# Performance work log

Measured on AMD Instinct MI355X. Metric: run time of the kernel, lower is better.

The kernel has to match this reference:

```python
import jax, jax.numpy as jnp
import numpy as np

EMBED = 1024
HEADS = 16
HEAD_DIM = EMBED // HEADS
FFN_DIM = 4096
SEQ = 2048
BATCH = 2
EPS = 1e-5


def setup_inputs() -> dict:
    key = jax.random.key(0)
    ks = jax.random.split(key, 13)
    s = lambda n: 1.0 / np.sqrt(n)
    return {
        "x": jax.random.normal(ks[0], (BATCH, SEQ, EMBED), jnp.float32),
        # qkv projection (stored as [in, out])
        "w_qkv": jax.random.normal(ks[1], (EMBED, 3 * EMBED), jnp.float32) * s(EMBED),
        "b_qkv": jax.random.normal(ks[2], (3 * EMBED,), jnp.float32) * 0.02,
        "w_out": jax.random.normal(ks[3], (EMBED, EMBED), jnp.float32) * s(EMBED),
        "b_out": jax.random.normal(ks[4], (EMBED,), jnp.float32) * 0.02,
        # FFN
        "w_up": jax.random.normal(ks[5], (EMBED, FFN_DIM), jnp.float32) * s(EMBED),
        "b_up": jax.random.normal(ks[6], (FFN_DIM,), jnp.float32) * 0.02,
        "w_down": jax.random.normal(ks[7], (FFN_DIM, EMBED), jnp.float32) * s(FFN_DIM),
        "b_down": jax.random.normal(ks[8], (EMBED,), jnp.float32) * 0.02,
        # LayerNorms
        "g1": jnp.ones((EMBED,), jnp.float32),
        "be1": jnp.zeros((EMBED,), jnp.float32),
        "g2": jnp.ones((EMBED,), jnp.float32),
        "be2": jnp.zeros((EMBED,), jnp.float32),
    }


def _layernorm(x, g, b):
    mu = jnp.mean(x, axis=-1, keepdims=True)
    var = jnp.mean(jnp.square(x - mu), axis=-1, keepdims=True)
    return (x - mu) * jax.lax.rsqrt(var + EPS) * g + b


def reference(x, w_qkv, b_qkv, w_out, b_out, w_up, b_up, w_down, b_down, g1, be1, g2, be2):
    B, S, E = x.shape
    qkv = (x @ w_qkv + b_qkv).reshape(B, S, 3, HEADS, HEAD_DIM)
    qkv = jnp.transpose(qkv, (2, 0, 3, 1, 4))
    q, k, v = qkv[0], qkv[1], qkv[2]
    scale = 1.0 / jnp.sqrt(jnp.float32(HEAD_DIM))
    attn = jnp.einsum("bhqd,bhkd->bhqk", q, k) * scale  # [B,H,S,S]
    causal = jnp.tril(jnp.ones((S, S), bool))
    attn = jnp.where(causal, attn, -jnp.inf)
    attn = jax.nn.softmax(attn, axis=-1)
    out = jnp.einsum("bhqk,bhkd->bhqd", attn, v)  # [B,H,S,D]
    out = jnp.transpose(out, (0, 2, 1, 3)).reshape(B, S, E)
    attn_out = out @ w_out + b_out
    x = _layernorm(x + attn_out, g1, be1)
    ffn_out = jax.nn.relu(x @ w_up + b_up) @ w_down + b_down
    return _layernorm(x + ffn_out, g2, be2)
```

## Files before the change

### kernel.cpp

```cpp
#include <hip/hip_runtime.h>
#include <hip/hip_bf16.h>

#define EMBED 1024
#define HEADS 16
#define HDIM 64
#define FFN 4096
#define SEQ 2048
#define BATCH 2
#define MTOT (BATCH*SEQ)
#define QSCALE 0.1803368801111137f

typedef __attribute__((ext_vector_type(8))) short bf16x8;
typedef __attribute__((ext_vector_type(4))) float f32x4;
typedef __attribute__((ext_vector_type(16))) float f32x16;
typedef unsigned short u16;
typedef unsigned int u32;

__device__ __forceinline__ u16 f2bf(float f) {
  union { float f; unsigned u; } v; v.f = f;
  unsigned r = v.u + 0x7FFFu + ((v.u >> 16) & 1u);
  return (u16)(r >> 16);
}

__device__ __forceinline__ void async_ld16(const void* g, void* l) {
  __builtin_amdgcn_global_load_lds((const __attribute__((address_space(1))) void*)g,
                                   (__attribute__((address_space(3))) void*)l,
                                   16, 0, 0);
}

__global__ __launch_bounds__(256) void k_cvt(const float* __restrict__ in,
                                             u16* __restrict__ out, int n4) {
  int i = blockIdx.x * 256 + threadIdx.x;
  int st = gridDim.x * 256;
  for (; i < n4; i += st) {
    float4 v = ((const float4*)in)[i];
    ushort4 o;
    o.x = f2bf(v.x); o.y = f2bf(v.y); o.z = f2bf(v.z); o.w = f2bf(v.w);
    ((ushort4*)out)[i] = o;
  }
}

__global__ __launch_bounds__(256) void k_tr(const float* __restrict__ w,
                                            u16* __restrict__ wT, int K, int N) {
  __shared__ u16 tile[32][33];
  int n0 = blockIdx.x * 32, k0 = blockIdx.y * 32;
  int tx = threadIdx.x, ty = threadIdx.y;
  #pragma unroll
  for (int i = 0; i < 4; ++i) {
    int k = k0 + ty + i * 8;
    tile[ty + i * 8][tx] = f2bf(w[(size_t)k * N + n0 + tx]);
  }
  __syncthreads();
  #pragma unroll
  for (int i = 0; i < 4; ++i) {
    int n = n0 + ty + i * 8;
    wT[(size_t)n * K + k0 + tx] = tile[tx][ty + i * 8];
  }
}

__global__ __launch_bounds__(256) void k_vtr(const u16* __restrict__ V,
                                             u16* __restrict__ Vt) {
  __shared__ u16 t[64][72];
  const int s0 = blockIdx.x * 64;
  const size_t ib = (size_t)blockIdx.y * (size_t)SEQ * HDIM;
  const size_t ob = (size_t)blockIdx.y * (size_t)HDIM * SEQ;
  const int tid = threadIdx.x;
  const int r = tid >> 2, c0 = (tid & 3) * 16;
  bf16x8 v0 = *(const bf16x8*)(V + ib + (size_t)(s0 + r) * HDIM + c0);
  bf16x8 v1 = *(const bf16x8*)(V + ib + (size_t)(s0 + r) * HDIM + c0 + 8);
  #pragma unroll
  for (int j = 0; j < 8; ++j) {
    t[c0 + j][r] = (u16)v0[j];
    t[c0 + 8 + j][r] = (u16)v1[j];
  }
  __syncthreads();
  const int d = tid >> 2, sc = (tid & 3) * 16;
  bf16x8 o0, o1;
  #pragma unroll
  for (int j = 0; j < 8; ++j) { o0[j] = t[d][sc + j]; o1[j] = t[d][sc + 8 + j]; }
  *(bf16x8*)(Vt + ob + (size_t)d * SEQ + s0 + sc) = o0;
  *(bf16x8*)(Vt + ob + (size_t)d * SEQ + s0 + sc + 8) = o1;
}

template <int OMODE, bool RELU>
__global__ __launch_bounds__(512) void k_gemm8(
    const u16* __restrict__ A, const u16* __restrict__ BT,
    const float* __restrict__ bias,
    void* __restrict__ out0, void* __restrict__ out1, void* __restrict__ out2,
    int M, int N, int K) {
  __shared__ __align__(16) u16 As[2][2][128 * 64];
  __shared__ __align__(16) u16 Bs[2][2][128 * 64];
  const int tid = threadIdx.x;
  const int lane = tid & 63, g = lane >> 4, li = lane & 15;
  const int wid = tid >> 6, wm = wid >> 2, wn = wid & 3;

  const int gx = gridDim.x;
  const int nwg = gx * gridDim.y;
  const int flat = blockIdx.y * gx + blockIdx.x;
  const int cpx = nwg >> 3;
  const int swz = (flat & 7) * cpx + (flat >> 3);
  const int m0 = (swz / gx) * 256, n0 = (swz % gx) * 256;

  f32x4 acc[8][4] = {};

  const u16* Ablk = A + (size_t)m0 * K;
  const u16* Bblk = BT + (size_t)n0 * K;
  const int trow = tid >> 3;
  const int sc = (tid & 7) ^ (trow & 7);

  auto stageA = [&](int buf, int h, int kt) {
    #pragma unroll
    for (int r = 0; r < 2; ++r)
      async_ld16(Ablk + (size_t)(h * 64 + r * 128 + trow) * K + kt + sc * 8,
                 &As[buf][h][0] + r * 4096 + tid * 8);
  };
  auto stageB = [&](int buf, int h, int kt) {
    #pragma unroll
    for (int r = 0; r < 2; ++r) {
      const int p = trow + r * 64;
      async_ld16(Bblk + (size_t)(((p >> 5) << 6) + h * 32 + (p & 31)) * K + kt + sc * 8,
                 &Bs[buf][h][0] + r * 4096 + tid * 8);
    }
  };

#define VM4_ asm volatile("s_waitcnt vmcnt(4)" ::: "memory")
#define VM2_ asm volatile("s_waitcnt vmcnt(2)" ::: "memory")
#define VM0_ asm volatile("s_waitcnt vmcnt(0)" ::: "memory")
#define VMN_
#define GP8(IH, JH, VMSTMT, STAGE_STMT) do {                                   \
    bf16x8 a_[4][2], b_[2][2];                                                 \
    _Pragma("unroll")                                                          \
    for (int i2 = 0; i2 < 4; ++i2) {                                           \
      const int pa = wm * 64 + i2 * 16 + li;                                   \
      _Pragma("unroll")                                                        \
      for (int ks = 0; ks < 2; ++ks)                                           \
        a_[i2][ks] = *(const bf16x8*)(&As[cur][IH][0] + pa * 64 +              \
                                      (((ks * 4 + g) ^ (li & 7)) * 8));        \
    }                                                                          \
    _Pragma("unroll")                                                          \
    for (int j2 = 0; j2 < 2; ++j2) {                                           \
      const int pb = wn * 32 + j2 * 16 + li;                                   \
      _Pragma("unroll")                                                        \
      for (int ks = 0; ks < 2; ++ks)                                           \
        b_[j2][ks] = *(const bf16x8*)(&Bs[cur][JH][0] + pb * 64 +              \
                                      (((ks * 4 + g) ^ (li & 7)) * 8));        \
    }                                                                          \
    STAGE_STMT;                                                                \
    VMSTMT;                                                                    \
    __builtin_amdgcn_s_barrier();                                              \
    asm volatile("s_waitcnt lgkmcnt(0)" ::: "memory");                         \
    __builtin_amdgcn_sched_barrier(0);                                         \
    __builtin_amdgcn_s_setprio(1);                                             \
    _Pragma("unroll")                                                          \
    for (int ks = 0; ks < 2; ++ks)                                             \
      _Pragma("unroll")                                                        \
      for (int i2 = 0; i2 < 4; ++i2)                                           \
        _Pragma("unroll")                                                      \
        for (int j2 = 0; j2 < 2; ++j2)                                         \
          acc[IH * 4 + i2][JH * 2 + j2] = __builtin_amdgcn_mfma_f32_16x16x32_bf16( \
              a_[i2][ks], b_[j2][ks], acc[IH * 4 + i2][JH * 2 + j2], 0, 0, 0); \
    __builtin_amdgcn_s_setprio(0);                                             \
    __builtin_amdgcn_s_barrier();                                              \
    asm volatile("" ::: "memory");                                             \
  } while (0)

  stageA(0, 0, 0); stageB(0, 0, 0); stageA(0, 1, 0); stageB(0, 1, 0);
  VM4_;
  __builtin_amdgcn_s_barrier();
  asm volatile("" ::: "memory");

  int cur = 0;
  const int nkt = K >> 6;
  for (int t = 0; t < nkt - 1; ++t) {
    const int kn = (t + 1) * 64;
    GP8(0, 0, VM4_, stageA(cur ^ 1, 0, kn));
    GP8(1, 0, VM4_, stageB(cur ^ 1, 0, kn));
    GP8(0, 1, VMN_, stageA(cur ^ 1, 1, kn));
    GP8(1, 1, VM4_, stageB(cur ^ 1, 1, kn));
    cur ^= 1;
  }
  GP8(0, 0, VM2_, );
  GP8(1, 0, VM0_, );
  GP8(0, 1, VMN_, );
  GP8(1, 1, VMN_, );
#undef GP8
#undef VM4_
#undef VM2_
#undef VM0_
#undef VMN_

  float bcol[4];
  #pragma unroll
  for (int j = 0; j < 4; ++j) bcol[j] = bias[n0 + wn * 64 + j * 16 + li];

  #pragma unroll
  for (int i = 0; i < 8; ++i) {
    #pragma unroll
    for (int j = 0; j < 4; ++j) {
      #pragma unroll
      for (int r = 0; r < 4; ++r) {
        int row = m0 + wm * 128 + i * 16 + g * 4 + r;
        int col = n0 + wn * 64 + j * 16 + li;
        float v = acc[i][j][r] + bcol[j];
        if (RELU) v = fmaxf(v, 0.f);
        if (OMODE == 0) {
          ((u16*)out0)[(size_t)row * N + col] = f2bf(v);
        } else {
          int which = col >> 10, hh = (col >> 6) & 15, d = col & 63;
          int bb = row >> 11, ss = row & 2047;
          if (which == 0) v *= QSCALE;
          u16* dst = which == 0 ? (u16*)out0 : (which == 1 ? (u16*)out1 : (u16*)out2);
          dst[((size_t)((bb * 16 + hh) * 2048 + ss)) * 64 + d] = f2bf(v);
        }
      }
    }
  }
}

template <int BN, int BK, int OMODE, bool RELU>
__global__ __launch_bounds__(256) void k_gemm(
    const u16* __restrict__ A, const u16* __restrict__ BT,
    const float* __restrict__ bias,
    void* __restrict__ out0, void* __restrict__ out1, void* __restrict__ out2,
    int M, int N, int K) {
  constexpr int NR = BN / 32;
  constexpr int KS = BK / 32;
  constexpr int TPR = BK / 8;
  constexpr int RPI = 256 / TPR;
  constexpr int CM = TPR - 1;

  __shared__ u16 As[2][128 * BK];
  __shared__ u16 Bs[2][BN * BK];
  const int tid = threadIdx.x;
  const int lane = tid & 63, g = lane >> 4, li = lane & 15;
  const int wid = tid >> 6, wm = wid >> 1, wn = wid & 1;

  const int gx = gridDim.x;
  const int nwg = gx * gridDim.y;
  const int flat = blockIdx.y * gx + blockIdx.x;
  const int cpx = nwg >> 3;
  const int swz = (flat & 7) * cpx + (flat >> 3);
  const int m0 = (swz / gx) * 128, n0 = (swz % gx) * BN;

  f32x4 acc[4][NR] = {};

  const u16* Ablk = A + (size_t)m0 * K;
  const u16* Bblk = BT + (size_t)n0 * K;
  const int srow = tid / TPR;
  const int scol = ((tid % TPR) ^ (srow & CM)) * 8;

  auto stage = [&](int buf, int kt) {
    #pragma unroll
    for (int r = 0; r < 128; r += RPI)
      async_ld16(Ablk + (size_t)(srow + r) * K + kt + scol, &As[buf][(srow + r) * BK] + (tid % TPR) * 8);
    #pragma unroll
    for (int r = 0; r < BN; r += RPI)
      async_ld16(Bblk + (size_t)(srow + r) * K + kt + scol, &Bs[buf][(srow + r) * BK] + (tid % TPR) * 8);
  };

  stage(0, 0);
  int cur = 0;
  for (int kt = 0; kt < K; kt += BK) {
    __syncthreads();
    if (kt + BK < K) stage(cur ^ 1, kt + BK);

    bf16x8 af[4][KS], bfr[NR][KS];
    #pragma unroll
    for (int i = 0; i < 4; ++i) {
      const int row = wm * 64 + i * 16 + li;
      #pragma unroll
      for (int ks = 0; ks < KS; ++ks) {
        const int c = ks * 4 + g;
        af[i][ks] = *(const bf16x8*)(&As[cur][row * BK] + ((c ^ (row & CM)) & CM) * 8);
      }
    }
    #pragma unroll
    for (int j = 0; j < NR; ++j) {
      const int row = wn * (BN / 2) + j * 16 + li;
      #pragma unroll
      for (int ks = 0; ks < KS; ++ks) {
        const int c = ks * 4 + g;
        bfr[j][ks] = *(const bf16x8*)(&Bs[cur][row * BK] + ((c ^ (row & CM)) & CM) * 8);
      }
    }
    #pragma unroll
    for (int ks = 0; ks < KS; ++ks)
      #pragma unroll
      for (int i = 0; i < 4; ++i)
        #pragma unroll
        for (int j = 0; j < NR; ++j)
          acc[i][j] = __builtin_amdgcn_mfma_f32_16x16x32_bf16(af[i][ks], bfr[j][ks], acc[i][j], 0, 0, 0);
    cur ^= 1;
  }

  float bcol[NR];
  #pragma unroll
  for (int j = 0; j < NR; ++j) bcol[j] = bias[n0 + wn * (BN / 2) + j * 16 + li];

  #pragma unroll
  for (int i = 0; i < 4; ++i) {
    #pragma unroll
    for (int j = 0; j < NR; ++j) {
      #pragma unroll
      for (int r = 0; r < 4; ++r) {
        int row = m0 + wm * 64 + i * 16 + g * 4 + r;
        int col = n0 + wn * (BN / 2) + j * 16 + li;
        float v = acc[i][j][r] + bcol[j];
        if (RELU) v = fmaxf(v, 0.f);
        if (OMODE == 0) {
          ((u16*)out0)[(size_t)row * N + col] = f2bf(v);
        } else if (OMODE == 1) {
          ((float*)out0)[(size_t)row * N + col] = v;
        } else {
          int which = col >> 10, hh = (col >> 6) & 15, d = col & 63;
          int bb = row >> 11, ss = row & 2047;
          if (which == 0) v *= QSCALE;
          u16* dst = which == 0 ? (u16*)out0 : (which == 1 ? (u16*)out1 : (u16*)out2);
          dst[((size_t)((bb * 16 + hh) * 2048 + ss)) * 64 + d] = f2bf(v);
        }
      }
    }
  }
}

__global__ __launch_bounds__(256, 3) void k_attn6(
    const u16* __restrict__ Q, const u16* __restrict__ K,
    const u16* __restrict__ Vt, u16* __restrict__ ctx) {
  const int bh = blockIdx.x;
  const int t32 = 63 - (int)blockIdx.y;
  const int b = bh >> 4, h = bh & 15;
  const int tid = threadIdx.x;
  const int wid = tid >> 6, lane = tid & 63;
  const int ql = lane & 31, hl = lane >> 5;

  __shared__ __align__(16) float mrg[3][64][34];

  const int wq0 = t32 * 32;
  const int qg = wq0 + ql;
  const int nt = ((wq0 + 31) >> 6) + 1;

  const size_t kbase = (size_t)bh * SEQ * HDIM;
  const size_t vbase = (size_t)bh * HDIM * SEQ;

  bf16x8 qf[4];
  #pragma unroll
  for (int d4 = 0; d4 < 4; ++d4)
    qf[d4] = *(const bf16x8*)(Q + kbase + (size_t)qg * HDIM + d4 * 16 + hl * 8);

  const u16* kp = K + kbase + (size_t)ql * HDIM + hl * 8;
  const u16* vp = Vt + vbase + (size_t)ql * SEQ + hl * 8;

  f32x16 o0 = {}, o1 = {};
  float m_run = -1e30f, l_run = 0.f;

  for (int kt = wid; kt < nt; kt += 4) {
    const bool kh1 = (kt * 64 + 32 <= wq0 + 31);
    const bool domask = (kt * 64 + (kh1 ? 63 : 31) > wq0);
    const int koff = kt * 64 * HDIM;

    bf16x8 kf0[4], kf1[4];
    #pragma unroll
    for (int d4 = 0; d4 < 4; ++d4) {
      kf0[d4] = *(const bf16x8*)(kp + koff + d4 * 16);
      if (kh1) kf1[d4] = *(const bf16x8*)(kp + koff + 32 * HDIM + d4 * 16);
    }
    bf16x8 vf0[4], vf1[4];
    #pragma unroll
    for (int t = 0; t < 4; ++t)
      if (t < 2 || kh1) {
        vf0[t] = *(const bf16x8*)(vp + kt * 64 + t * 16);
        vf1[t] = *(const bf16x8*)(vp + 32 * SEQ + kt * 64 + t * 16);
      }

    f32x16 S0 = {}, S1 = {};
    #pragma unroll
    for (int d4 = 0; d4 < 4; ++d4)
      S0 = __builtin_amdgcn_mfma_f32_32x32x16_bf16(kf0[d4], qf[d4], S0, 0, 0, 0);
    if (kh1) {
      #pragma unroll
      for (int d4 = 0; d4 < 4; ++d4)
        S1 = __builtin_amdgcn_mfma_f32_32x32x16_bf16(kf1[d4], qf[d4], S1, 0, 0, 0);
    }

    if (domask) {
      const int qrel = qg - kt * 64 - 4 * hl;
      #pragma unroll
      for (int r = 0; r < 16; ++r) {
        const int kc = (r & 3) + 8 * (r >> 2);
        S0[r] = (kc <= qrel) ? S0[r] : -3.0e38f;
      }
      if (kh1) {
        #pragma unroll
        for (int r = 0; r < 16; ++r) {
          const int kc = 32 + (r & 3) + 8 * (r >> 2);
          S1[r] = (kc <= qrel) ? S1[r] : -3.0e38f;
        }
      }
    }

    float mt = -3.0e38f;
    #pragma unroll
    for (int r = 0; r < 16; ++r) mt = fmaxf(mt, S0[r]);
    if (kh1) {
      #pragma unroll
      for (int r = 0; r < 16; ++r) mt = fmaxf(mt, S1[r]);
    }
    mt = fmaxf(mt, __shfl_xor(mt, 32, 64));

    if (!__all(mt <= m_run + 8.0f)) {
      const float mn = fmaxf(m_run, mt);
      const float alpha = exp2f(m_run - mn);
      l_run *= alpha;
      o0 *= alpha;
      o1 *= alpha;
      m_run = mn;
    }
    float sum = 0.f;
    #pragma unroll
    for (int r = 0; r < 16; ++r) { S0[r] = exp2f(S0[r] - m_run); sum += S0[r]; }
    if (kh1) {
      #pragma unroll
      for (int r = 0; r < 16; ++r) { S1[r] = exp2f(S1[r] - m_run); sum += S1[r]; }
    }
    sum += __shfl_xor(sum, 32, 64);
    l_run += sum;

    u32 pk[2][8], sw[2][8];
    #pragma unroll
    for (int m = 0; m < 4; ++m) {
      asm("v_cvt_pk_bf16_f32 %0, %1, %2" : "=v"(pk[0][2*m])   : "v"(S0[4*m+0]), "v"(S0[4*m+1]));
      asm("v_cvt_pk_bf16_f32 %0, %1, %2" : "=v"(pk[0][2*m+1]) : "v"(S0[4*m+2]), "v"(S0[4*m+3]));
    }
    #pragma unroll
    for (int i = 0; i < 8; ++i) sw[0][i] = __shfl_xor(pk[0][i], 32, 64);
    if (kh1) {
      #pragma unroll
      for (int m = 0; m < 4; ++m) {
        asm("v_cvt_pk_bf16_f32 %0, %1, %2" : "=v"(pk[1][2*m])   : "v"(S1[4*m+0]), "v"(S1[4*m+1]));
        asm("v_cvt_pk_bf16_f32 %0, %1, %2" : "=v"(pk[1][2*m+1]) : "v"(S1[4*m+2]), "v"(S1[4*m+3]));
      }
      #pragma unroll
      for (int i = 0; i < 8; ++i) sw[1][i] = __shfl_xor(pk[1][i], 32, 64);
    }

    #pragma unroll
    for (int t = 0; t < 4; ++t) {
      if (t < 2 || kh1) {
        const int c = t >> 1, m0 = 2 * (t & 1), m1 = m0 + 1;
        union { u32 u[4]; bf16x8 v; } pf;
        pf.u[0] = hl ? sw[c][2*m1]   : pk[c][2*m0];
        pf.u[1] = hl ? sw[c][2*m1+1] : pk[c][2*m0+1];
        pf.u[2] = hl ? pk[c][2*m1]   : sw[c][2*m0];
        pf.u[3] = hl ? pk[c][2*m1+1] : sw[c][2*m0+1];
        o0 = __builtin_amdgcn_mfma_f32_32x32x16_bf16(vf0[t], pf.v, o0, 0, 0, 0);
        o1 = __builtin_amdgcn_mfma_f32_32x32x16_bf16(vf1[t], pf.v, o1, 0, 0, 0);
      }
    }
  }

  if (wid > 0) {
    float* p = &mrg[wid - 1][lane][0];
    *(f32x16*)(p) = o0;
    *(f32x16*)(p + 16) = o1;
    p[32] = m_run;
    p[33] = l_run;
  }
  __syncthreads();
  if (wid > 0) return;

  float M = m_run;
  #pragma unroll
  for (int w = 0; w < 3; ++w) M = fmaxf(M, mrg[w][lane][32]);
  const float fa = exp2f(m_run - M);
  f32x16 acc0 = o0 * fa, acc1 = o1 * fa;
  float L = l_run * fa;
  #pragma unroll
  for (int w = 0; w < 3; ++w) {
    const float* p = &mrg[w][lane][0];
    const float fw = exp2f(p[32] - M);
    L += p[33] * fw;
    f32x16 t0 = *(const f32x16*)(p);
    f32x16 t1 = *(const f32x16*)(p + 16);
    acc0 += t0 * fw;
    acc1 += t1 * fw;
  }
  const float inv = 1.f / L;

  u16* outp = ctx + (size_t)(b * SEQ + qg) * EMBED + h * HDIM + 4 * hl;
  #pragma unroll
  for (int m = 0; m < 4; ++m) {
    ushort4 s0v, s1v;
    s0v.x = f2bf(acc0[4*m+0] * inv); s0v.y = f2bf(acc0[4*m+1] * inv);
    s0v.z = f2bf(acc0[4*m+2] * inv); s0v.w = f2bf(acc0[4*m+3] * inv);
    *(ushort4*)(outp + 8 * m) = s0v;
    s1v.x = f2bf(acc1[4*m+0] * inv); s1v.y = f2bf(acc1[4*m+1] * inv);
    s1v.z = f2bf(acc1[4*m+2] * inv); s1v.w = f2bf(acc1[4*m+3] * inv);
    *(ushort4*)(outp + 32 + 8 * m) = s1v;
  }
}

__global__ __launch_bounds__(256) void k_add_ln(
    const float* __restrict__ a, const float* __restrict__ bmat,
    const float* __restrict__ gam, const float* __restrict__ bet,
    float* __restrict__ outf, u16* __restrict__ outb) {
  const int row = blockIdx.x;
  const int t = threadIdx.x;
  __shared__ float red[8];
  float4 va = ((const float4*)(a + (size_t)row * EMBED))[t];
  float4 vb = ((const float4*)(bmat + (size_t)row * EMBED))[t];
  float s0 = va.x + vb.x, s1 = va.y + vb.y, s2 = va.z + vb.z, s3 = va.w + vb.w;
  float sum = s0 + s1 + s2 + s3;
  float sq = s0 * s0 + s1 * s1 + s2 * s2 + s3 * s3;
  #pragma unroll
  for (int m = 1; m < 64; m <<= 1) {
    sum += __shfl_xor(sum, m, 64);
    sq += __shfl_xor(sq, m, 64);
  }
  int wid = t >> 6;
  if ((t & 63) == 0) { red[wid] = sum; red[4 + wid] = sq; }
  __syncthreads();
  sum = red[0] + red[1] + red[2] + red[3];
  sq = red[4] + red[5] + red[6] + red[7];
  float mean = sum * (1.f / EMBED);
  float var = sq * (1.f / EMBED) - mean * mean;
  float rstd = rsqrtf(var + 1e-5f);
  float4 gv = ((const float4*)gam)[t], bev = ((const float4*)bet)[t];
  float y0 = (s0 - mean) * rstd * gv.x + bev.x;
  float y1 = (s1 - mean) * rstd * gv.y + bev.y;
  float y2 = (s2 - mean) * rstd * gv.z + bev.z;
  float y3 = (s3 - mean) * rstd * gv.w + bev.w;
  float4 o; o.x = y0; o.y = y1; o.z = y2; o.w = y3;
  ((float4*)(outf + (size_t)row * EMBED))[t] = o;
  if (outb) {
    ushort4 ob; ob.x = f2bf(y0); ob.y = f2bf(y1); ob.z = f2bf(y2); ob.w = f2bf(y3);
    ((ushort4*)(outb + (size_t)row * EMBED))[t] = ob;
  }
}

extern "C" void kernel_launch(void* const* d_in, const int* in_sizes, int n_in,
                              void* d_out, int out_size, void* d_ws, size_t ws_size,
                              hipStream_t stream) {
  const float* x      = (const float*)d_in[0];
  const float* w_qkv  = (const float*)d_in[1];
  const float* b_qkv  = (const float*)d_in[2];
  const float* w_out  = (const float*)d_in[3];
  const float* b_out  = (const float*)d_in[4];
  const float* w_up   = (const float*)d_in[5];
  const float* b_up   = (const float*)d_in[6];
  const float* w_down = (const float*)d_in[7];
  const float* b_down = (const float*)d_in[8];
  const float* g1  = (const float*)d_in[9];
  const float* be1 = (const float*)d_in[10];
  const float* g2  = (const float*)d_in[11];
  const float* be2 = (const float*)d_in[12];

  char* ws = (char*)d_ws;
  size_t off = 0;
  auto alloc = [&](size_t bytes) { void* p = ws + off; off += (bytes + 255) & ~(size_t)255; return p; };

  u16* xb     = (u16*)alloc((size_t)MTOT * EMBED * 2);
  u16* wqkvT  = (u16*)alloc((size_t)3 * EMBED * EMBED * 2);
  u16* woutT  = (u16*)alloc((size_t)EMBED * EMBED * 2);
  u16* wupT   = (u16*)alloc((size_t)FFN * EMBED * 2);
  u16* wdownT = (u16*)alloc((size_t)EMBED * FFN * 2);
  u16* qb     = (u16*)alloc((size_t)MTOT * EMBED * 2);
  u16* kb     = (u16*)alloc((size_t)MTOT * EMBED * 2);
  u16* vb     = (u16*)alloc((size_t)MTOT * EMBED * 2);
  u16* vtb    = (u16*)alloc((size_t)MTOT * EMBED * 2);
  u16* ctx    = (u16*)alloc((size_t)MTOT * EMBED * 2);
  float* attn_proj = (float*)alloc((size_t)MTOT * EMBED * 4);
  float* y_f32     = (float*)alloc((size_t)MTOT * EMBED * 4);
  u16* y_bf16      = (u16*)alloc((size_t)MTOT * EMBED * 2);
  u16* hmid        = (u16*)alloc((size_t)MTOT * FFN * 2);
  float* ffn_o     = (float*)alloc((size_t)MTOT * EMBED * 4);

  dim3 trb(32, 8);
  k_cvt<<<2048, 256, 0, stream>>>(x, xb, MTOT * EMBED / 4);
  k_tr<<<dim3(3 * EMBED / 32, EMBED / 32), trb, 0, stream>>>(w_qkv, wqkvT, EMBED, 3 * EMBED);
  k_tr<<<dim3(EMBED / 32, EMBED / 32), trb, 0, stream>>>(w_out, woutT, EMBED, EMBED);
  k_tr<<<dim3(FFN / 32, EMBED / 32), trb, 0, stream>>>(w_up, wupT, EMBED, FFN);
  k_tr<<<dim3(EMBED / 32, FFN / 32), trb, 0, stream>>>(w_down, wdownT, FFN, EMBED);

  k_gemm8<2, false><<<dim3(3 * EMBED / 256, MTOT / 256), 512, 0, stream>>>(
      xb, wqkvT, b_qkv, qb, kb, vb, MTOT, 3 * EMBED, EMBED);

  k_vtr<<<dim3(SEQ / 64, BATCH * HEADS), 256, 0, stream>>>(vb, vtb);

  k_attn6<<<dim3(BATCH * HEADS, 64), 256, 0, stream>>>(qb, kb, vtb, ctx);

  k_gemm<64, 64, 1, false><<<dim3(EMBED / 64, MTOT / 128), 256, 0, stream>>>(
      ctx, woutT, b_out, attn_proj, nullptr, nullptr, MTOT, EMBED, EMBED);

  k_add_ln<<<MTOT, 256, 0, stream>>>(x, attn_proj, g1, be1, y_f32, y_bf16);

  k_gemm8<0, true><<<dim3(FFN / 256, MTOT / 256), 512, 0, stream>>>(
      y_bf16, wupT, b_up, hmid, nullptr, nullptr, MTOT, FFN, EMBED);

  k_gemm<64, 64, 1, false><<<dim3(EMBED / 64, MTOT / 128), 256, 0, stream>>>(
      hmid, wdownT, b_down, ffn_o, nullptr, nullptr, MTOT, EMBED, FFN);

  k_add_ln<<<MTOT, 256, 0, stream>>>(y_f32, ffn_o, g2, be2, (float*)d_out, nullptr);

  (void)in_sizes; (void)n_in; (void)out_size; (void)ws_size;
}
```

Measured before the change: 266.9 us.

## Write Q/K/V in MFMA fragment-packed layout from QKV GEMM, drop V transpose kernel

The QKV GEMM epilogue now scatters Q, K and V directly into a pre-packed layout matching the attention kernel's MFMA fragment order, with V already transposed. This removes the separate V-transpose kernel and makes each lane's fragment load in attention a contiguous 512-element block per wave, giving fully coalesced loads. The cost is a more scattered, costlier store pattern in the GEMM epilogue.

After: 241.4 us. 1.11x faster.

```diff
diff --git a/kernel.cpp b/kernel.cpp
--- a/kernel.cpp
+++ b/kernel.cpp
@@ -26,6 +26,27 @@
   __builtin_amdgcn_global_load_lds((const __attribute__((address_space(1))) void*)g,
                                    (__attribute__((address_space(3))) void*)l,
                                    16, 0, 0);
+}
+
+__device__ __forceinline__ void qkv_scatter(u16* qp, u16* kp, u16* vp,
+                                            int row, int col, float v) {
+  const int which = col >> 10, hh = (col >> 6) & 15, d = col & 63;
+  const int bb = row >> 11, ss = row & 2047;
+  const int bh = bb * 16 + hh;
+  if (which == 0) {
+    v *= QSCALE;
+    size_t idx = ((((size_t)bh * 64 + (ss >> 5)) * 4 + (d >> 4)) << 9)
+               + (((ss & 31) + 32 * ((d >> 3) & 1)) << 3) + (d & 7);
+    qp[idx] = f2bf(v);
+  } else if (which == 1) {
+    size_t idx = ((((size_t)bh * 32 + (ss >> 6)) * 8 + (d >> 4) * 2 + ((ss >> 5) & 1)) << 9)
+               + (((ss & 31) + 32 * ((d >> 3) & 1)) << 3) + (d & 7);
+    kp[idx] = f2bf(v);
+  } else {
+    size_t idx = ((((size_t)bh * 32 + (ss >> 6)) * 8 + ((ss & 63) >> 4) * 2 + (d >> 5)) << 9)
+               + (((d & 31) + 32 * ((ss >> 3) & 1)) << 3) + (ss & 7);
+    vp[idx] = f2bf(v);
+  }
 }
 
 __global__ __launch_bounds__(256) void k_cvt(const float* __restrict__ in,
@@ -56,30 +77,6 @@
     int n = n0 + ty + i * 8;
     wT[(size_t)n * K + k0 + tx] = tile[tx][ty + i * 8];
   }
-}
-
-__global__ __launch_bounds__(256) void k_vtr(const u16* __restrict__ V,
-                                             u16* __restrict__ Vt) {
-  __shared__ u16 t[64][72];
-  const int s0 = blockIdx.x * 64;
-  const size_t ib = (size_t)blockIdx.y * (size_t)SEQ * HDIM;
-  const size_t ob = (size_t)blockIdx.y * (size_t)HDIM * SEQ;
-  const int tid = threadIdx.x;
-  const int r = tid >> 2, c0 = (tid & 3) * 16;
-  bf16x8 v0 = *(const bf16x8*)(V + ib + (size_t)(s0 + r) * HDIM + c0);
-  bf16x8 v1 = *(const bf16x8*)(V + ib + (size_t)(s0 + r) * HDIM + c0 + 8);
-  #pragma unroll
-  for (int j = 0; j < 8; ++j) {
-    t[c0 + j][r] = (u16)v0[j];
-    t[c0 + 8 + j][r] = (u16)v1[j];
-  }
-  __syncthreads();
-  const int d = tid >> 2, sc = (tid & 3) * 16;
-  bf16x8 o0, o1;
-  #pragma unroll
-  for (int j = 0; j < 8; ++j) { o0[j] = t[d][sc + j]; o1[j] = t[d][sc + 8 + j]; }
-  *(bf16x8*)(Vt + ob + (size_t)d * SEQ + s0 + sc) = o0;
-  *(bf16x8*)(Vt + ob + (size_t)d * SEQ + s0 + sc + 8) = o1;
 }
 
 template <int OMODE, bool RELU>
@@ -206,11 +203,7 @@
         if (OMODE == 0) {
           ((u16*)out0)[(size_t)row * N + col] = f2bf(v);
         } else {
-          int which = col >> 10, hh = (col >> 6) & 15, d = col & 63;
-          int bb = row >> 11, ss = row & 2047;
-          if (which == 0) v *= QSCALE;
-          u16* dst = which == 0 ? (u16*)out0 : (which == 1 ? (u16*)out1 : (u16*)out2);
-          dst[((size_t)((bb * 16 + hh) * 2048 + ss)) * 64 + d] = f2bf(v);
+          qkv_scatter((u16*)out0, (u16*)out1, (u16*)out2, row, col, v);
         }
       }
     }
@@ -312,20 +305,16 @@
         } else if (OMODE == 1) {
           ((float*)out0)[(size_t)row * N + col] = v;
         } else {
-          int which = col >> 10, hh = (col >> 6) & 15, d = col & 63;
-          int bb = row >> 11, ss = row & 2047;
-          if (which == 0) v *= QSCALE;
-          u16* dst = which == 0 ? (u16*)out0 : (which == 1 ? (u16*)out1 : (u16*)out2);
-          dst[((size_t)((bb * 16 + hh) * 2048 + ss)) * 64 + d] = f2bf(v);
+          qkv_scatter((u16*)out0, (u16*)out1, (u16*)out2, row, col, v);
         }
       }
     }
   }
 }
 
-__global__ __launch_bounds__(256, 3) void k_attn6(
-    const u16* __restrict__ Q, const u16* __restrict__ K,
-    const u16* __restrict__ Vt, u16* __restrict__ ctx) {
+__global__ __launch_bounds__(256, 3) void k_attn7(
+    const u16* __restrict__ Qp, const u16* __restrict__ Kp,
+    const u16* __restrict__ Vp, u16* __restrict__ ctx) {
   const int bh = blockIdx.x;
   const int t32 = 63 - (int)blockIdx.y;
   const int b = bh >> 4, h = bh & 15;
@@ -339,16 +328,16 @@
   const int qg = wq0 + ql;
   const int nt = ((wq0 + 31) >> 6) + 1;
 
-  const size_t kbase = (size_t)bh * SEQ * HDIM;
-  const size_t vbase = (size_t)bh * HDIM * SEQ;
-
   bf16x8 qf[4];
-  #pragma unroll
-  for (int d4 = 0; d4 < 4; ++d4)
-    qf[d4] = *(const bf16x8*)(Q + kbase + (size_t)qg * HDIM + d4 * 16 + hl * 8);
-
-  const u16* kp = K + kbase + (size_t)ql * HDIM + hl * 8;
-  const u16* vp = Vt + vbase + (size_t)ql * SEQ + hl * 8;
+  {
+    const u16* qpb = Qp + ((((size_t)bh * 64 + t32) * 4) << 9) + lane * 8;
+    #pragma unroll
+    for (int d4 = 0; d4 < 4; ++d4)
+      qf[d4] = *(const bf16x8*)(qpb + (d4 << 9));
+  }
+
+  const u16* kbase = Kp + (((size_t)bh * 32) << 12) + lane * 8;
+  const u16* vbase = Vp + (((size_t)bh * 32) << 12) + lane * 8;
 
   f32x16 o0 = {}, o1 = {};
   float m_run = -1e30f, l_run = 0.f;
@@ -356,20 +345,21 @@
   for (int kt = wid; kt < nt; kt += 4) {
     const bool kh1 = (kt * 64 + 32 <= wq0 + 31);
     const bool domask = (kt * 64 + (kh1 ? 63 : 31) > wq0);
-    const int koff = kt * 64 * HDIM;
+    const u16* kb_ = kbase + ((size_t)kt << 12);
+    const u16* vb_ = vbase + ((size_t)kt << 12);
 
     bf16x8 kf0[4], kf1[4];
     #pragma unroll
     for (int d4 = 0; d4 < 4; ++d4) {
-      kf0[d4] = *(const bf16x8*)(kp + koff + d4 * 16);
-      if (kh1) kf1[d4] = *(const bf16x8*)(kp + koff + 32 * HDIM + d4 * 16);
+      kf0[d4] = *(const bf16x8*)(kb_ + ((d4 * 2 + 0) << 9));
+      if (kh1) kf1[d4] = *(const bf16x8*)(kb_ + ((d4 * 2 + 1) << 9));
     }
     bf16x8 vf0[4], vf1[4];
     #pragma unroll
     for (int t = 0; t < 4; ++t)
       if (t < 2 || kh1) {
-        vf0[t] = *(const bf16x8*)(vp + kt * 64 + t * 16);
-        vf1[t] = *(const bf16x8*)(vp + 32 * SEQ + kt * 64 + t * 16);
+        vf0[t] = *(const bf16x8*)(vb_ + ((t * 2 + 0) << 9));
+        vf1[t] = *(const bf16x8*)(vb_ + ((t * 2 + 1) << 9));
       }
 
     f32x16 S0 = {}, S1 = {};
@@ -563,10 +553,9 @@
   u16* woutT  = (u16*)alloc((size_t)EMBED * EMBED * 2);
   u16* wupT   = (u16*)alloc((size_t)FFN * EMBED * 2);
   u16* wdownT = (u16*)alloc((size_t)EMBED * FFN * 2);
-  u16* qb     = (u16*)alloc((size_t)MTOT * EMBED * 2);
-  u16* kb     = (u16*)alloc((size_t)MTOT * EMBED * 2);
-  u16* vb     = (u16*)alloc((size_t)MTOT * EMBED * 2);
-  u16* vtb    = (u16*)alloc((size_t)MTOT * EMBED * 2);
+  u16* qp     = (u16*)alloc((size_t)MTOT * EMBED * 2);
+  u16* kp     = (u16*)alloc((size_t)MTOT * EMBED * 2);
+  u16* vp     = (u16*)alloc((size_t)MTOT * EMBED * 2);
   u16* ctx    = (u16*)alloc((size_t)MTOT * EMBED * 2);
   float* attn_proj = (float*)alloc((size_t)MTOT * EMBED * 4);
   float* y_f32     = (float*)alloc((size_t)MTOT * EMBED * 4);
@@ -582,11 +571,9 @@
   k_tr<<<dim3(EMBED / 32, FFN / 32), trb, 0, stream>>>(w_down, wdownT, FFN, EMBED);
 
   k_gemm8<2, false><<<dim3(3 * EMBED / 256, MTOT / 256), 512, 0, stream>>>(
-      xb, wqkvT, b_qkv, qb, kb, vb, MTOT, 3 * EMBED, EMBED);
-
-  k_vtr<<<dim3(SEQ / 64, BATCH * HEADS), 256, 0, stream>>>(vb, vtb);
-
-  k_attn6<<<dim3(BATCH * HEADS, 64), 256, 0, stream>>>(qb, kb, vtb, ctx);
+      xb, wqkvT, b_qkv, qp, kp, vp, MTOT, 3 * EMBED, EMBED);
+
+  k_attn7<<<dim3(BATCH * HEADS, 64), 256, 0, stream>>>(qp, kp, vp, ctx);
 
   k_gemm<64, 64, 1, false><<<dim3(EMBED / 64, MTOT / 128), 256, 0, stream>>>(
       ctx, woutT, b_out, attn_proj, nullptr, nullptr, MTOT, EMBED, EMBED);
```
